# Optimization experiments

Hardware: AMD Instinct MI355X
Metric: run time of the kernel (lower is better)

The kernel has to match this reference:

```python
import math
import jax, jax.numpy as jnp
import numpy as np

RS_IN = [(128, 0), (64, 1), (32, 2)]
RS_OUT = [(128, 0), (64, 1), (32, 2)]
SET_LF = [0, 1, 2, 3, 4]
BATCH = 512
HIDDEN = 64

def _lfilters(l_in, l_out):
    return list(range(abs(l_in - l_out), l_in + l_out + 1))

N_PATH = sum(mo * mi * len(_lfilters(li, lo)) for mo, lo in RS_OUT for mi, li in RS_IN)  # 70656

# ---------- Clebsch-Gordan (numpy, setup time only) ----------

def _su2_cg(j1, j2, j3):
    f = math.factorial
    C = np.zeros((2 * j1 + 1, 2 * j2 + 1, 2 * j3 + 1))
    for m1 in range(-j1, j1 + 1):
        for m2 in range(-j2, j2 + 1):
            m3 = m1 + m2
            if abs(m3) > j3:
                continue
            pref = math.sqrt((2 * j3 + 1) * f(j3 + j1 - j2) * f(j3 - j1 + j2) * f(j1 + j2 - j3) / f(j1 + j2 + j3 + 1))
            pref *= math.sqrt(f(j3 + m3) * f(j3 - m3) * f(j1 - m1) * f(j1 + m1) * f(j2 - m2) * f(j2 + m2))
            s = 0.0
            for v in range(0, j1 + j2 - j3 + 1):
                d = [v, j1 + j2 - j3 - v, j1 - m1 - v, j2 + m2 - v, j3 - j2 + m1 + v, j3 - j1 - m2 + v]
                if any(x < 0 for x in d):
                    continue
                s += (-1) ** v / float(np.prod([f(x) for x in d]))
            C[j1 + m1, j2 + m2, j3 + m3] = pref * s
    return C

def _r2c(l):
    # change of basis real -> complex spherical harmonics, with phase making CG real
    q = np.zeros((2 * l + 1, 2 * l + 1), dtype=complex)
    for m in range(-l, 0):
        q[l + m, l + abs(m)] = 1 / math.sqrt(2)
        q[l + m, l - abs(m)] = -1j / math.sqrt(2)
    q[l, l] = 1
    for m in range(1, l + 1):
        q[l + m, l + abs(m)] = (-1) ** m / math.sqrt(2)
        q[l + m, l - abs(m)] = 1j * (-1) ** m / math.sqrt(2)
    return ((-1j) ** l) * q

def _cg_real(l1, l2, l3):
    C = np.einsum('ai,bj,ck,abc->ijk', _r2c(l1), _r2c(l2), np.conj(_r2c(l3)), _su2_cg(l1, l2, l3))
    C = C.imag if np.abs(C.imag).sum() > np.abs(C.real).sum() else C.real
    n = np.linalg.norm(C)
    return C / n if n > 0 else C

# ---------- real spherical harmonics (jax) ----------

def _sh(ls, r):
    # r: [batch, 3] -> Y: [sum(2l+1 for l in ls), batch]
    eps = 1e-9
    nrm = jnp.linalg.norm(r, axis=1, keepdims=True)
    d = r / jnp.maximum(nrm, eps)
    x, y, z = d[:, 0], d[:, 1], d[:, 2]
    rxy = jnp.sqrt(jnp.maximum(x * x + y * y, eps * eps))
    cphi, sphi = x / rxy, y / rxy
    lmax = max(ls)
    somx2 = jnp.sqrt(jnp.maximum(1.0 - z * z, 1e-12))
    P = {}
    pmm = jnp.ones_like(z)
    for m in range(lmax + 1):
        if m > 0:
            pmm = pmm * (2 * m - 1) * somx2
        P[(m, m)] = pmm
        if m + 1 <= lmax:
            P[(m + 1, m)] = z * (2 * m + 1) * pmm
        for l in range(m + 2, lmax + 1):
            P[(l, m)] = ((2 * l - 1) * z * P[(l - 1, m)] - (l + m - 1) * P[(l - 2, m)]) / (l - m)
    cm = [jnp.ones_like(z), cphi]
    sm = [jnp.zeros_like(z), sphi]
    for m in range(2, lmax + 1):
        cm.append(cm[m - 1] * cphi - sm[m - 1] * sphi)
        sm.append(sm[m - 1] * cphi + cm[m - 1] * sphi)
    f = math.factorial
    rows = []
    for l in ls:
        for m in range(-l, l + 1):
            am = abs(m)
            N = math.sqrt((2 * l + 1) / (4 * math.pi) * f(l - am) / f(l + am))
            if m == 0:
                rows.append(N * P[(l, 0)])
            elif m > 0:
                rows.append(math.sqrt(2) * N * P[(l, am)] * cm[am])
            else:
                rows.append(math.sqrt(2) * N * P[(l, am)] * sm[am])
    return jnp.stack(rows, axis=0)

# ---------- kernel forward ----------

def _kernel_forward(r, w1, b1, w2, b2, Qs):
    batch = r.shape[0]
    Ys = _sh(SET_LF, r)                       # [25, batch]
    radii = jnp.linalg.norm(r, axis=1)        # [batch]
    h = jax.nn.relu(radii[:, None] @ w1 + b1) # [batch, HIDDEN]
    coefficients = h @ w2 + b2                # [batch, N_PATH]
    begin_c = 0
    out_blocks = []
    for i, (mul_out, l_out) in enumerate(RS_OUT):
        num_summed = sum(mul_in * len(_lfilters(l_in, l_out)) for mul_in, l_in in RS_IN)
        in_blocks = []
        for j, (mul_in, l_in) in enumerate(RS_IN):
            lfs = _lfilters(l_in, l_out)
            n = mul_out * mul_in * len(lfs)
            c = coefficients[:, begin_c:begin_c + n].reshape(batch, mul_out, mul_in, len(lfs))
            begin_c += n
            Qij = Qs[i][j]
            K = 0
            for k, lf in enumerate(lfs):
                off_y = sum(2 * l + 1 for l in SET_LF if l < lf)
                Y = Ys[off_y:off_y + 2 * lf + 1]                 # [2lf+1, batch]
                off_q = sum(2 * l + 1 for l in lfs if l < lf)
                Q = Qij[:, :, off_q:off_q + 2 * lf + 1]          # [2lo+1, 2li+1, 2lf+1]
                K = K + jnp.einsum('ijk,kz,zuv->zuivj', Q, Y, c[..., k])
            # normalization == 'norm'
            xnorm = math.sqrt(2 * l_in + 1) * math.sqrt(4 * math.pi) / math.sqrt(num_summed)
            K = K * xnorm
            in_blocks.append(K.reshape(batch, mul_out * (2 * l_out + 1), mul_in * (2 * l_in + 1)))
        out_blocks.append(jnp.concatenate(in_blocks, axis=2))
    return jnp.concatenate(out_blocks, axis=1)  # [batch, 480, 480]

def setup_inputs() -> dict:
    key = jax.random.key(0)
    ks = jax.random.split(key, 5)
    inp = {}
    inp['r'] = jax.random.normal(ks[0], (BATCH, 3), dtype=jnp.float32)
    inp['w1'] = jax.random.normal(ks[1], (1, HIDDEN), dtype=jnp.float32) * 0.5
    inp['b1'] = jax.random.normal(ks[2], (HIDDEN,), dtype=jnp.float32) * 0.1
    inp['w2'] = jax.random.normal(ks[3], (HIDDEN, N_PATH), dtype=jnp.float32) * (1.0 / math.sqrt(HIDDEN))
    inp['b2'] = jax.random.normal(ks[4], (N_PATH,), dtype=jnp.float32) * 0.01
    for i, (mo, lo) in enumerate(RS_OUT):
        for j, (mi, li) in enumerate(RS_IN):
            Q = np.concatenate([_cg_real(lo, li, lf) for lf in _lfilters(li, lo)], axis=2)
            inp['Q_%d_%d' % (i, j)] = jnp.asarray(Q, dtype=jnp.float32)
    return inp

def reference(r, w1, b1, w2, b2, Q_0_0, Q_0_1, Q_0_2, Q_1_0, Q_1_1, Q_1_2, Q_2_0, Q_2_1, Q_2_2):
    Qs = [[Q_0_0, Q_0_1, Q_0_2], [Q_1_0, Q_1_1, Q_1_2], [Q_2_0, Q_2_1, Q_2_2]]
    return _kernel_forward(r, w1, b1, w2, b2, Qs)
```

## Files before the change

kernel.cpp:

```cpp
#include <hip/hip_runtime.h>
#include <math.h>

#define NPATH 70656
#define NBATCH 512
#define OUTD 480
#define OUTSZ (OUTD*OUTD)
#define ZCHV 64
#define ZT 8

constexpr int CBEG_TAB[9] = {0,16384,24576,28672,36864,49152,55296,59392,65536};

struct QPtrs { const float* q[9]; };

__global__ __launch_bounds__(256) void sh_mlp_kernel(
    const float* __restrict__ r, const float* __restrict__ w1,
    const float* __restrict__ b1, float* __restrict__ Yg,
    float* __restrict__ hTz)
{
  int z = blockIdx.x*256 + threadIdx.x;
  if (z >= NBATCH) return;
  float x = r[3*z], y = r[3*z+1], zz = r[3*z+2];
  float nrm = sqrtf(x*x + y*y + zz*zz);
  float inv = 1.0f / fmaxf(nrm, 1e-9f);
  float dx = x*inv, dy = y*inv, dz = zz*inv;
  float rxy = sqrtf(fmaxf(dx*dx + dy*dy, 1e-18f));
  float cphi = dx/rxy, sphi = dy/rxy;
  float somx2 = sqrtf(fmaxf(1.0f - dz*dz, 1e-12f));

  float P[5][5];
  float pmm = 1.0f;
  #pragma unroll
  for (int m = 0; m < 5; ++m) {
    if (m > 0) pmm *= (float)(2*m-1) * somx2;
    P[m][m] = pmm;
    if (m+1 < 5) P[m+1][m] = dz * (float)(2*m+1) * pmm;
    #pragma unroll
    for (int l = m+2; l < 5; ++l)
      P[l][m] = ((float)(2*l-1)*dz*P[l-1][m] - (float)(l+m-1)*P[l-2][m]) / (float)(l-m);
  }
  float cm[5], sm[5];
  cm[0]=1.0f; sm[0]=0.0f; cm[1]=cphi; sm[1]=sphi;
  #pragma unroll
  for (int m = 2; m < 5; ++m) {
    cm[m] = cm[m-1]*cphi - sm[m-1]*sphi;
    sm[m] = sm[m-1]*cphi + cm[m-1]*sphi;
  }
  const float fact[9] = {1,1,2,6,24,120,720,5040,40320};
  int row = 0;
  #pragma unroll
  for (int l = 0; l < 5; ++l) {
    #pragma unroll
    for (int m = -l; m <= l; ++m) {
      int am = m < 0 ? -m : m;
      float N = sqrtf((float)(2*l+1) / 12.566370614359172f * fact[l-am] / fact[l+am]);
      float v;
      if (m == 0)      v = N * P[l][0];
      else if (m > 0)  v = 1.4142135623730951f * N * P[l][am] * cm[am];
      else             v = 1.4142135623730951f * N * P[l][am] * sm[am];
      Yg[z*25 + row] = v;
      ++row;
    }
  }
  #pragma unroll
  for (int k = 0; k < 64; ++k)
    hTz[z*64 + k] = fmaxf(nrm * w1[k] + b1[k], 0.0f);
}

template<int LO, int LI>
__device__ __forceinline__ void stream_body(
    int bidl, const float* __restrict__ Yg, const float* __restrict__ hTz,
    const float* __restrict__ w2f, const float* __restrict__ b2,
    const float* __restrict__ Q, float* __restrict__ out)
{
  constexpr int DI = 2*LO+1, DJ = 2*LI+1;
  constexpr int MI = 128>>LI;
  constexpr int NUV = (128>>LO)*MI;
  constexpr int UVB = NUV/256;
  constexpr int LF = LO+LI;
  constexpr int MAXM = 2*LF+1;
  constexpr int ROWOFF = (LO==0)?0:((LO==1)?128:320);
  constexpr int COLOFF = (LI==0)?0:((LI==1)?128:320);
  constexpr int CBEG = CBEG_TAB[LO*3+LI];
  constexpr float NS = (LO==0)?224.0f:((LO==1)?416.0f:480.0f);
  const float xn = sqrtf((float)(2*LI+1) * 12.566370614359172f / NS);

  const int tid = threadIdx.x;
  const int uvb   = bidl % UVB;
  const int chunk = bidl / UVB;
  const int z0 = chunk * ZCHV;
  const int uv = uvb*256 + tid;
  const int uu = uv >> (7-LI);
  const int vv = uv & (MI-1);
  const int path = CBEG + uv;
  const float b2p = b2[path];

  float Qv[DI*DJ][MAXM];
  #pragma unroll
  for (int ij = 0; ij < DI*DJ; ++ij)
    #pragma unroll
    for (int m = 0; m < MAXM; ++m)
      Qv[ij][m] = Q[ij*MAXM + m];

  float* outR = out + (size_t)(ROWOFF + uu*DI)*OUTD + COLOFF + vv*DJ;

  for (int t0 = 0; t0 < ZCHV; t0 += ZT) {
    float acc[ZT];
    #pragma unroll
    for (int zt = 0; zt < ZT; ++zt) acc[zt] = b2p;
    #pragma unroll
    for (int kk = 0; kk < 64; kk += 16) {
      float w2c[16];
      #pragma unroll
      for (int k = 0; k < 16; ++k) w2c[k] = w2f[(size_t)(kk+k)*NPATH + path];
      #pragma unroll
      for (int zt = 0; zt < ZT; ++zt) {
        const float* hz = hTz + (size_t)(z0+t0+zt)*64 + kk;
        float s0=0.f, s1=0.f, s2=0.f, s3=0.f;
        #pragma unroll
        for (int k = 0; k < 16; k += 4) {
          s0 = fmaf(hz[k],   w2c[k],   s0);
          s1 = fmaf(hz[k+1], w2c[k+1], s1);
          s2 = fmaf(hz[k+2], w2c[k+2], s2);
          s3 = fmaf(hz[k+3], w2c[k+3], s3);
        }
        acc[zt] += (s0+s1)+(s2+s3);
      }
    }
    #pragma unroll
    for (int zt = 0; zt < ZT; ++zt) {
      const int z = z0 + t0 + zt;
      const float* yz = Yg + (size_t)z*25 + LF*LF;
      const float c = acc[zt]*xn;
      float* oz = outR + (size_t)z*OUTSZ;
      #pragma unroll
      for (int i = 0; i < DI; ++i)
        #pragma unroll
        for (int j = 0; j < DJ; ++j) {
          float a = 0.0f;
          #pragma unroll
          for (int m = 0; m < MAXM; ++m) a = fmaf(Qv[i*DJ+j][m], yz[m], a);
          oz[i*OUTD + j] = a*c;
        }
    }
  }
}

template<int LO, int LI>
__device__ __forceinline__ void tiled_body(
    int bidl, const float* __restrict__ Yg, const float* __restrict__ hTz,
    const float* __restrict__ w2f, const float* __restrict__ b2,
    const float* __restrict__ Q, float* __restrict__ out,
    float* c_lds, float* A_lds)
{
  constexpr int DI = 2*LO+1, DJ = 2*LI+1;
  constexpr int MO = 128>>LO, MI = 128>>LI;
  constexpr int NL = 2*((LO<LI)?LO:LI)+1;
  constexpr int LF0 = (LO>LI)?(LO-LI):(LI-LO);
  constexpr int QDIM = (LO+LI+1)*(LO+LI+1) - LF0*LF0;
  constexpr int NUV = MO*MI;
  constexpr int G = 256/NL;
  constexpr int UVB = (NUV + G - 1)/G;
  constexpr int NOUT = G*DI*DJ;
  constexpr int OPT = (NOUT + 255)/256;
  constexpr int ASIZE = DI*DJ*NL;
  constexpr int MAXM = 2*(LO+LI)+1;
  constexpr int ROWOFF = (LO==0)?0:((LO==1)?128:320);
  constexpr int COLOFF = (LI==0)?0:((LI==1)?128:320);
  constexpr int CBEG = CBEG_TAB[LO*3+LI];
  constexpr float NS = (LO==0)?224.0f:((LO==1)?416.0f:480.0f);
  const float xn = sqrtf((float)(2*LI+1) * 12.566370614359172f / NS);

  const int tid = threadIdx.x;
  const int uvb   = bidl % UVB;
  const int chunk = bidl / UVB;
  const int uv0 = uvb * G;
  const int z0  = chunk * ZCHV;

  const int gl = tid / NL;
  const int kf = tid % NL;
  const bool cact = (gl < G) && (uv0 + gl < NUV);
  const int path = CBEG + (cact ? ((uv0+gl)*NL + kf) : 0);
  const float b2p = b2[path];

  float Qv[MAXM];
  int yb = 0;
  {
    int t = (tid < ASIZE) ? tid : 0;
    int i  = t / (DJ*NL);
    int j  = (t / NL) % DJ;
    int kA = t % NL;
    int lf = LF0 + kA;
    int qoff = kA*(2*LF0 + kA);
    int mlim = 2*lf + 1;
    yb = lf*lf;
    #pragma unroll
    for (int m = 0; m < MAXM; ++m)
      Qv[m] = (m < mlim) ? Q[(i*DJ + j)*QDIM + qoff + m] : 0.0f;
  }

  int rowoff_o[OPT], aidx_o[OPT], cidx_o[OPT];
  bool val_o[OPT];
  #pragma unroll
  for (int t = 0; t < OPT; ++t) {
    int o = tid + 256*t;
    bool v = o < NOUT;
    int oo = v ? o : 0;
    int i   = oo / (G*DJ);
    int rem = oo % (G*DJ);
    int g   = rem / DJ;
    int j   = rem % DJ;
    int uv  = uv0 + g;
    v = v && (uv < NUV);
    int uu = uv >> (7-LI);
    int vv = uv & (MI-1);
    rowoff_o[t] = (uu*DI + i)*OUTD + vv*DJ + j;
    aidx_o[t] = (i*DJ + j)*NL;
    cidx_o[t] = g*NL;
    val_o[t] = v;
  }

  float* outR = out + ROWOFF*OUTD + COLOFF;

  for (int tile = 0; tile < ZCHV/ZT; ++tile) {
    const int p = tile & 1;
    float* cb = c_lds + p*(ZT*256);
    float* ab = A_lds + p*(ZT*128);
    const int zb = z0 + tile*ZT;

    float acc[ZT];
    #pragma unroll
    for (int zt = 0; zt < ZT; ++zt) acc[zt] = b2p;
    #pragma unroll
    for (int kk = 0; kk < 64; kk += 16) {
      float w2c[16];
      #pragma unroll
      for (int k = 0; k < 16; ++k) w2c[k] = w2f[(size_t)(kk+k)*NPATH + path];
      #pragma unroll
      for (int zt = 0; zt < ZT; ++zt) {
        const float* hz = hTz + (size_t)(zb+zt)*64 + kk;
        float s0=0.f, s1=0.f, s2=0.f, s3=0.f;
        #pragma unroll
        for (int k = 0; k < 16; k += 4) {
          s0 = fmaf(hz[k],   w2c[k],   s0);
          s1 = fmaf(hz[k+1], w2c[k+1], s1);
          s2 = fmaf(hz[k+2], w2c[k+2], s2);
          s3 = fmaf(hz[k+3], w2c[k+3], s3);
        }
        acc[zt] += (s0+s1)+(s2+s3);
      }
    }
    #pragma unroll
    for (int zt = 0; zt < ZT; ++zt) cb[zt*256 + tid] = acc[zt];

    if (tid < ASIZE) {
      #pragma unroll
      for (int zt = 0; zt < ZT; ++zt) {
        const float* yz = Yg + (size_t)(zb+zt)*25 + yb;
        float s = 0.0f;
        #pragma unroll
        for (int m = 0; m < MAXM; ++m) s = fmaf(Qv[m], yz[m], s);
        ab[zt*128 + tid] = s;
      }
    }
    __syncthreads();

    for (int zt = 0; zt < ZT; ++zt) {
      float* oz = outR + (size_t)(zb+zt)*OUTSZ;
      const float* cbz = cb + zt*256;
      const float* abz = ab + zt*128;
      #pragma unroll
      for (int t = 0; t < OPT; ++t) {
        if (val_o[t]) {
          float s = 0.0f;
          #pragma unroll
          for (int k = 0; k < NL; ++k) s += abz[aidx_o[t] + k] * cbz[cidx_o[t] + k];
          oz[rowoff_o[t]] = s*xn;
        }
      }
    }
  }
}

__global__ __launch_bounds__(256) void tp_stream_kernel(
    const float* __restrict__ Yg, const float* __restrict__ hTz,
    const float* __restrict__ w2, const float* __restrict__ b2,
    QPtrs qp, float* __restrict__ out)
{
  const int b = blockIdx.x;
  const int chunk = b / 160;
  const int r = b % 160;
  if      (r <  64) stream_body<0,0>(chunk*64 + r,      Yg,hTz,w2,b2,qp.q[0],out);
  else if (r <  96) stream_body<0,1>(chunk*32 + (r- 64),Yg,hTz,w2,b2,qp.q[1],out);
  else if (r < 112) stream_body<0,2>(chunk*16 + (r- 96),Yg,hTz,w2,b2,qp.q[2],out);
  else if (r < 144) stream_body<1,0>(chunk*32 + (r-112),Yg,hTz,w2,b2,qp.q[3],out);
  else              stream_body<2,0>(chunk*16 + (r-144),Yg,hTz,w2,b2,qp.q[6],out);
}

__global__ __launch_bounds__(256) void tp_tiled_kernel(
    const float* __restrict__ Yg, const float* __restrict__ hTz,
    const float* __restrict__ w2, const float* __restrict__ b2,
    QPtrs qp, float* __restrict__ out)
{
  __shared__ float c_lds[2*ZT*256];
  __shared__ float A_lds[2*ZT*128];
  const int b = blockIdx.x;
  const int chunk = b / 120;
  const int r = b % 120;
  if      (r <  49) tiled_body<1,1>(chunk*49 + r,      Yg,hTz,w2,b2,qp.q[4],out,c_lds,A_lds);
  else if (r <  74) tiled_body<1,2>(chunk*25 + (r-49), Yg,hTz,w2,b2,qp.q[5],out,c_lds,A_lds);
  else if (r <  99) tiled_body<2,1>(chunk*25 + (r-74), Yg,hTz,w2,b2,qp.q[7],out,c_lds,A_lds);
  else              tiled_body<2,2>(chunk*21 + (r-99), Yg,hTz,w2,b2,qp.q[8],out,c_lds,A_lds);
}

extern "C" void kernel_launch(void* const* d_in, const int* in_sizes, int n_in,
                              void* d_out, int out_size, void* d_ws, size_t ws_size,
                              hipStream_t stream)
{
  (void)in_sizes; (void)n_in; (void)out_size; (void)ws_size;
  const float* r  = (const float*)d_in[0];
  const float* w1 = (const float*)d_in[1];
  const float* b1 = (const float*)d_in[2];
  const float* w2 = (const float*)d_in[3];
  const float* b2 = (const float*)d_in[4];
  float* out = (float*)d_out;

  float* ws  = (float*)d_ws;
  float* Yg  = ws;
  float* hTz = ws + 12800;

  QPtrs qp;
  for (int i = 0; i < 9; ++i) qp.q[i] = (const float*)d_in[5 + i];

  const int nchunk = NBATCH / ZCHV;
  hipLaunchKernelGGL(sh_mlp_kernel, dim3(2), dim3(256), 0, stream, r, w1, b1, Yg, hTz);
  hipLaunchKernelGGL(tp_tiled_kernel,  dim3(nchunk*120), dim3(256), 0, stream,
                     Yg, hTz, w2, b2, qp, out);
  hipLaunchKernelGGL(tp_stream_kernel, dim3(nchunk*160), dim3(256), 0, stream,
                     Yg, hTz, w2, b2, qp, out);
}
```

Measured before the change: 219.9 us.

## Transpose w2 per path, merge tensor-product kernels, double ZT tile

```diff
diff --git a/kernel.cpp b/kernel.cpp
--- a/kernel.cpp
+++ b/kernel.cpp
@@ -6,11 +6,32 @@
 #define OUTD 480
 #define OUTSZ (OUTD*OUTD)
 #define ZCHV 64
-#define ZT 8
+#define ZT 16
 
 constexpr int CBEG_TAB[9] = {0,16384,24576,28672,36864,49152,55296,59392,65536};
 
 struct QPtrs { const float* q[9]; };
+
+__global__ __launch_bounds__(256) void w2t_kernel(
+    const float* __restrict__ w2, float* __restrict__ w2T)
+{
+  __shared__ float tile[64][65];
+  const int p0 = blockIdx.x * 64;
+  const int tk = threadIdx.x >> 6;
+  const int tp = threadIdx.x & 63;
+  #pragma unroll
+  for (int kk = 0; kk < 64; kk += 4) {
+    int k = kk + tk;
+    tile[k][tp] = w2[(size_t)k*NPATH + p0 + tp];
+  }
+  __syncthreads();
+  #pragma unroll
+  for (int i = 0; i < 16; ++i) {
+    int idx = threadIdx.x + 256*i;
+    int pr = idx >> 6, kc = idx & 63;
+    w2T[(size_t)(p0 + pr)*64 + kc] = tile[kc][pr];
+  }
+}
 
 __global__ __launch_bounds__(256) void sh_mlp_kernel(
     const float* __restrict__ r, const float* __restrict__ w1,
@@ -69,7 +90,7 @@
 template<int LO, int LI>
 __device__ __forceinline__ void stream_body(
     int bidl, const float* __restrict__ Yg, const float* __restrict__ hTz,
-    const float* __restrict__ w2f, const float* __restrict__ b2,
+    const float* __restrict__ w2T, const float* __restrict__ b2,
     const float* __restrict__ Q, float* __restrict__ out)
 {
   constexpr int DI = 2*LO+1, DJ = 2*LI+1;
@@ -93,6 +114,7 @@
   const int vv = uv & (MI-1);
   const int path = CBEG + uv;
   const float b2p = b2[path];
+  const float4* w2p4 = (const float4*)(w2T + (size_t)path*64);
 
   float Qv[DI*DJ][MAXM];
   #pragma unroll
@@ -110,8 +132,10 @@
     #pragma unroll
     for (int kk = 0; kk < 64; kk += 16) {
       float w2c[16];
-      #pragma unroll
-      for (int k = 0; k < 16; ++k) w2c[k] = w2f[(size_t)(kk+k)*NPATH + path];
+      *(float4*)&w2c[0]  = w2p4[kk/4];
+      *(float4*)&w2c[4]  = w2p4[kk/4+1];
+      *(float4*)&w2c[8]  = w2p4[kk/4+2];
+      *(float4*)&w2c[12] = w2p4[kk/4+3];
       #pragma unroll
       for (int zt = 0; zt < ZT; ++zt) {
         const float* hz = hTz + (size_t)(z0+t0+zt)*64 + kk;
@@ -148,7 +172,7 @@
 template<int LO, int LI>
 __device__ __forceinline__ void tiled_body(
     int bidl, const float* __restrict__ Yg, const float* __restrict__ hTz,
-    const float* __restrict__ w2f, const float* __restrict__ b2,
+    const float* __restrict__ w2T, const float* __restrict__ b2,
     const float* __restrict__ Q, float* __restrict__ out,
     float* c_lds, float* A_lds)
 {
@@ -181,6 +205,7 @@
   const bool cact = (gl < G) && (uv0 + gl < NUV);
   const int path = CBEG + (cact ? ((uv0+gl)*NL + kf) : 0);
   const float b2p = b2[path];
+  const float4* w2p4 = (const float4*)(w2T + (size_t)path*64);
 
   float Qv[MAXM];
   int yb = 0;
@@ -222,10 +247,8 @@
   float* outR = out + ROWOFF*OUTD + COLOFF;
 
   for (int tile = 0; tile < ZCHV/ZT; ++tile) {
-    const int p = tile & 1;
-    float* cb = c_lds + p*(ZT*256);
-    float* ab = A_lds + p*(ZT*128);
     const int zb = z0 + tile*ZT;
+    __syncthreads();
 
     float acc[ZT];
     #pragma unroll
@@ -233,8 +256,10 @@
     #pragma unroll
     for (int kk = 0; kk < 64; kk += 16) {
       float w2c[16];
-      #pragma unroll
-      for (int k = 0; k < 16; ++k) w2c[k] = w2f[(size_t)(kk+k)*NPATH + path];
+      *(float4*)&w2c[0]  = w2p4[kk/4];
+      *(float4*)&w2c[4]  = w2p4[kk/4+1];
+      *(float4*)&w2c[8]  = w2p4[kk/4+2];
+      *(float4*)&w2c[12] = w2p4[kk/4+3];
       #pragma unroll
       for (int zt = 0; zt < ZT; ++zt) {
         const float* hz = hTz + (size_t)(zb+zt)*64 + kk;
@@ -250,7 +275,7 @@
       }
     }
     #pragma unroll
-    for (int zt = 0; zt < ZT; ++zt) cb[zt*256 + tid] = acc[zt];
+    for (int zt = 0; zt < ZT; ++zt) c_lds[zt*256 + tid] = acc[zt];
 
     if (tid < ASIZE) {
       #pragma unroll
@@ -259,15 +284,15 @@
         float s = 0.0f;
         #pragma unroll
         for (int m = 0; m < MAXM; ++m) s = fmaf(Qv[m], yz[m], s);
-        ab[zt*128 + tid] = s;
+        A_lds[zt*128 + tid] = s;
       }
     }
     __syncthreads();
 
     for (int zt = 0; zt < ZT; ++zt) {
       float* oz = outR + (size_t)(zb+zt)*OUTSZ;
-      const float* cbz = cb + zt*256;
-      const float* abz = ab + zt*128;
+      const float* cbz = c_lds + zt*256;
+      const float* abz = A_lds + zt*128;
       #pragma unroll
       for (int t = 0; t < OPT; ++t) {
         if (val_o[t]) {
@@ -281,35 +306,25 @@
   }
 }
 
-__global__ __launch_bounds__(256) void tp_stream_kernel(
+__global__ __launch_bounds__(256) void tp_kernel(
     const float* __restrict__ Yg, const float* __restrict__ hTz,
-    const float* __restrict__ w2, const float* __restrict__ b2,
+    const float* __restrict__ w2T, const float* __restrict__ b2,
     QPtrs qp, float* __restrict__ out)
 {
+  __shared__ float c_lds[ZT*256];
+  __shared__ float A_lds[ZT*128];
   const int b = blockIdx.x;
-  const int chunk = b / 160;
-  const int r = b % 160;
-  if      (r <  64) stream_body<0,0>(chunk*64 + r,      Yg,hTz,w2,b2,qp.q[0],out);
-  else if (r <  96) stream_body<0,1>(chunk*32 + (r- 64),Yg,hTz,w2,b2,qp.q[1],out);
-  else if (r < 112) stream_body<0,2>(chunk*16 + (r- 96),Yg,hTz,w2,b2,qp.q[2],out);
-  else if (r < 144) stream_body<1,0>(chunk*32 + (r-112),Yg,hTz,w2,b2,qp.q[3],out);
-  else              stream_body<2,0>(chunk*16 + (r-144),Yg,hTz,w2,b2,qp.q[6],out);
-}
-
-__global__ __launch_bounds__(256) void tp_tiled_kernel(
-    const float* __restrict__ Yg, const float* __restrict__ hTz,
-    const float* __restrict__ w2, const float* __restrict__ b2,
-    QPtrs qp, float* __restrict__ out)
-{
-  __shared__ float c_lds[2*ZT*256];
-  __shared__ float A_lds[2*ZT*128];
-  const int b = blockIdx.x;
-  const int chunk = b / 120;
-  const int r = b % 120;
-  if      (r <  49) tiled_body<1,1>(chunk*49 + r,      Yg,hTz,w2,b2,qp.q[4],out,c_lds,A_lds);
-  else if (r <  74) tiled_body<1,2>(chunk*25 + (r-49), Yg,hTz,w2,b2,qp.q[5],out,c_lds,A_lds);
-  else if (r <  99) tiled_body<2,1>(chunk*25 + (r-74), Yg,hTz,w2,b2,qp.q[7],out,c_lds,A_lds);
-  else              tiled_body<2,2>(chunk*21 + (r-99), Yg,hTz,w2,b2,qp.q[8],out,c_lds,A_lds);
+  const int chunk = b / 280;
+  const int r = b % 280;
+  if      (r <  64) stream_body<0,0>(chunk*64 + r,      Yg,hTz,w2T,b2,qp.q[0],out);
+  else if (r <  96) stream_body<0,1>(chunk*32 + (r- 64),Yg,hTz,w2T,b2,qp.q[1],out);
+  else if (r < 112) stream_body<0,2>(chunk*16 + (r- 96),Yg,hTz,w2T,b2,qp.q[2],out);
+  else if (r < 144) stream_body<1,0>(chunk*32 + (r-112),Yg,hTz,w2T,b2,qp.q[3],out);
+  else if (r < 160) stream_body<2,0>(chunk*16 + (r-144),Yg,hTz,w2T,b2,qp.q[6],out);
+  else if (r < 209) tiled_body<1,1>(chunk*49 + (r-160), Yg,hTz,w2T,b2,qp.q[4],out,c_lds,A_lds);
+  else if (r < 234) tiled_body<1,2>(chunk*25 + (r-209), Yg,hTz,w2T,b2,qp.q[5],out,c_lds,A_lds);
+  else if (r < 259) tiled_body<2,1>(chunk*25 + (r-234), Yg,hTz,w2T,b2,qp.q[7],out,c_lds,A_lds);
+  else              tiled_body<2,2>(chunk*21 + (r-259), Yg,hTz,w2T,b2,qp.q[8],out,c_lds,A_lds);
 }
 
 extern "C" void kernel_launch(void* const* d_in, const int* in_sizes, int n_in,
@@ -327,14 +342,13 @@
   float* ws  = (float*)d_ws;
   float* Yg  = ws;
   float* hTz = ws + 12800;
+  float* w2T = ws + 12800 + 32768;
 
   QPtrs qp;
   for (int i = 0; i < 9; ++i) qp.q[i] = (const float*)d_in[5 + i];
 
-  const int nchunk = NBATCH / ZCHV;
+  hipLaunchKernelGGL(w2t_kernel, dim3(NPATH/64), dim3(256), 0, stream, w2, w2T);
   hipLaunchKernelGGL(sh_mlp_kernel, dim3(2), dim3(256), 0, stream, r, w1, b1, Yg, hTz);
-  hipLaunchKernelGGL(tp_tiled_kernel,  dim3(nchunk*120), dim3(256), 0, stream,
-                     Yg, hTz, w2, b2, qp, out);
-  hipLaunchKernelGGL(tp_stream_kernel, dim3(nchunk*160), dim3(256), 0, stream,
-                     Yg, hTz, w2, b2, qp, out);
-}
+  hipLaunchKernelGGL(tp_kernel, dim3((NBATCH/ZCHV)*280), dim3(256), 0, stream,
+                     Yg, hTz, w2T, b2, qp, out);
+}
```

New measurement: 283.8 us. +29.1%, slower.

## Reorder w2 by filter-major layout and give each thread one uv with all filters

Applied to the files above, without the earlier changes.

```diff
diff --git a/kernel.cpp b/kernel.cpp
--- a/kernel.cpp
+++ b/kernel.cpp
@@ -5,12 +5,37 @@
 #define NBATCH 512
 #define OUTD 480
 #define OUTSZ (OUTD*OUTD)
-#define ZCHV 64
-#define ZT 8
+#define ZCHV_S 64
+#define ZTS 16
+#define ZCHV_T 16
+#define ZTT 8
 
 constexpr int CBEG_TAB[9] = {0,16384,24576,28672,36864,49152,55296,59392,65536};
+constexpr int NL_TAB[9]   = {1,1,1,1,3,3,1,3,5};
+constexpr int NUVL_TAB[9] = {14,13,12,13,12,11,12,11,10};
 
 struct QPtrs { const float* q[9]; };
+
+__global__ __launch_bounds__(256) void reorder_kernel(
+    const float* __restrict__ w2, const float* __restrict__ b2,
+    float* __restrict__ w2R, float* __restrict__ b2R)
+{
+  int p = blockIdx.x*256 + threadIdx.x;
+  if (p >= NPATH) return;
+  int reg = 0;
+  #pragma unroll
+  for (int i = 1; i < 9; ++i) if (p >= CBEG_TAB[i]) reg = i;
+  const int pl  = p - CBEG_TAB[reg];
+  const int nl  = NL_TAB[reg];
+  const int nuvl = NUVL_TAB[reg];
+  const int kf = pl >> nuvl;
+  const int uv = pl & ((1 << nuvl) - 1);
+  const int pold = CBEG_TAB[reg] + uv*nl + kf;
+  b2R[p] = b2[pold];
+  #pragma unroll 8
+  for (int k = 0; k < 64; ++k)
+    w2R[(size_t)k*NPATH + p] = w2[(size_t)k*NPATH + pold];
+}
 
 __global__ __launch_bounds__(256) void sh_mlp_kernel(
     const float* __restrict__ r, const float* __restrict__ w1,
@@ -69,7 +94,7 @@
 template<int LO, int LI>
 __device__ __forceinline__ void stream_body(
     int bidl, const float* __restrict__ Yg, const float* __restrict__ hTz,
-    const float* __restrict__ w2f, const float* __restrict__ b2,
+    const float* __restrict__ w2R, const float* __restrict__ b2R,
     const float* __restrict__ Q, float* __restrict__ out)
 {
   constexpr int DI = 2*LO+1, DJ = 2*LI+1;
@@ -87,12 +112,12 @@
   const int tid = threadIdx.x;
   const int uvb   = bidl % UVB;
   const int chunk = bidl / UVB;
-  const int z0 = chunk * ZCHV;
+  const int z0 = chunk * ZCHV_S;
   const int uv = uvb*256 + tid;
   const int uu = uv >> (7-LI);
   const int vv = uv & (MI-1);
   const int path = CBEG + uv;
-  const float b2p = b2[path];
+  const float b2p = b2R[path];
 
   float Qv[DI*DJ][MAXM];
   #pragma unroll
@@ -103,31 +128,35 @@
 
   float* outR = out + (size_t)(ROWOFF + uu*DI)*OUTD + COLOFF + vv*DJ;
 
-  for (int t0 = 0; t0 < ZCHV; t0 += ZT) {
-    float acc[ZT];
-    #pragma unroll
-    for (int zt = 0; zt < ZT; ++zt) acc[zt] = b2p;
+  for (int t0 = 0; t0 < ZCHV_S; t0 += ZTS) {
+    float acc[ZTS];
+    #pragma unroll
+    for (int zt = 0; zt < ZTS; ++zt) acc[zt] = b2p;
     #pragma unroll
     for (int kk = 0; kk < 64; kk += 16) {
       float w2c[16];
       #pragma unroll
-      for (int k = 0; k < 16; ++k) w2c[k] = w2f[(size_t)(kk+k)*NPATH + path];
-      #pragma unroll
-      for (int zt = 0; zt < ZT; ++zt) {
+      for (int k = 0; k < 16; ++k)
+        w2c[k] = w2R[(size_t)(kk+k)*NPATH + path];
+      #pragma unroll
+      for (int zt = 0; zt < ZTS; ++zt) {
         const float* hz = hTz + (size_t)(z0+t0+zt)*64 + kk;
+        float h[16];
+        #pragma unroll
+        for (int q = 0; q < 16; q += 4) *(float4*)&h[q] = *(const float4*)(hz+q);
         float s0=0.f, s1=0.f, s2=0.f, s3=0.f;
         #pragma unroll
         for (int k = 0; k < 16; k += 4) {
-          s0 = fmaf(hz[k],   w2c[k],   s0);
-          s1 = fmaf(hz[k+1], w2c[k+1], s1);
-          s2 = fmaf(hz[k+2], w2c[k+2], s2);
-          s3 = fmaf(hz[k+3], w2c[k+3], s3);
+          s0 = fmaf(h[k],   w2c[k],   s0);
+          s1 = fmaf(h[k+1], w2c[k+1], s1);
+          s2 = fmaf(h[k+2], w2c[k+2], s2);
+          s3 = fmaf(h[k+3], w2c[k+3], s3);
         }
         acc[zt] += (s0+s1)+(s2+s3);
       }
     }
     #pragma unroll
-    for (int zt = 0; zt < ZT; ++zt) {
+    for (int zt = 0; zt < ZTS; ++zt) {
       const int z = z0 + t0 + zt;
       const float* yz = Yg + (size_t)z*25 + LF*LF;
       const float c = acc[zt]*xn;
@@ -146,11 +175,10 @@
 }
 
 template<int LO, int LI>
-__device__ __forceinline__ void tiled_body(
+__device__ __forceinline__ void tiled_uv_body(
     int bidl, const float* __restrict__ Yg, const float* __restrict__ hTz,
-    const float* __restrict__ w2f, const float* __restrict__ b2,
-    const float* __restrict__ Q, float* __restrict__ out,
-    float* c_lds, float* A_lds)
+    const float* __restrict__ w2R, const float* __restrict__ b2R,
+    const float* __restrict__ Q, float* __restrict__ out, float* A_lds)
 {
   constexpr int DI = 2*LO+1, DJ = 2*LI+1;
   constexpr int MO = 128>>LO, MI = 128>>LI;
@@ -158,29 +186,27 @@
   constexpr int LF0 = (LO>LI)?(LO-LI):(LI-LO);
   constexpr int QDIM = (LO+LI+1)*(LO+LI+1) - LF0*LF0;
   constexpr int NUV = MO*MI;
-  constexpr int G = 256/NL;
-  constexpr int UVB = (NUV + G - 1)/G;
-  constexpr int NOUT = G*DI*DJ;
-  constexpr int OPT = (NOUT + 255)/256;
+  constexpr int UVB = NUV/256;
   constexpr int ASIZE = DI*DJ*NL;
   constexpr int MAXM = 2*(LO+LI)+1;
-  constexpr int ROWOFF = (LO==0)?0:((LO==1)?128:320);
-  constexpr int COLOFF = (LI==0)?0:((LI==1)?128:320);
+  constexpr int KKC = (NL==5)?8:16;
+  constexpr int ROWOFF = (LO==1)?128:320;
+  constexpr int COLOFF = (LI==1)?128:320;
   constexpr int CBEG = CBEG_TAB[LO*3+LI];
-  constexpr float NS = (LO==0)?224.0f:((LO==1)?416.0f:480.0f);
+  constexpr float NS = (LO==1)?416.0f:480.0f;
   const float xn = sqrtf((float)(2*LI+1) * 12.566370614359172f / NS);
 
   const int tid = threadIdx.x;
   const int uvb   = bidl % UVB;
   const int chunk = bidl / UVB;
-  const int uv0 = uvb * G;
-  const int z0  = chunk * ZCHV;
-
-  const int gl = tid / NL;
-  const int kf = tid % NL;
-  const bool cact = (gl < G) && (uv0 + gl < NUV);
-  const int path = CBEG + (cact ? ((uv0+gl)*NL + kf) : 0);
-  const float b2p = b2[path];
+  const int z0 = chunk * ZCHV_T;
+  const int uv = uvb*256 + tid;
+  const int uu = uv >> (7-LI);
+  const int vv = uv & (MI-1);
+
+  float b2p[NL];
+  #pragma unroll
+  for (int kf = 0; kf < NL; ++kf) b2p[kf] = b2R[CBEG + kf*NUV + uv];
 
   float Qv[MAXM];
   int yb = 0;
@@ -198,118 +224,95 @@
       Qv[m] = (m < mlim) ? Q[(i*DJ + j)*QDIM + qoff + m] : 0.0f;
   }
 
-  int rowoff_o[OPT], aidx_o[OPT], cidx_o[OPT];
-  bool val_o[OPT];
-  #pragma unroll
-  for (int t = 0; t < OPT; ++t) {
-    int o = tid + 256*t;
-    bool v = o < NOUT;
-    int oo = v ? o : 0;
-    int i   = oo / (G*DJ);
-    int rem = oo % (G*DJ);
-    int g   = rem / DJ;
-    int j   = rem % DJ;
-    int uv  = uv0 + g;
-    v = v && (uv < NUV);
-    int uu = uv >> (7-LI);
-    int vv = uv & (MI-1);
-    rowoff_o[t] = (uu*DI + i)*OUTD + vv*DJ + j;
-    aidx_o[t] = (i*DJ + j)*NL;
-    cidx_o[t] = g*NL;
-    val_o[t] = v;
-  }
-
-  float* outR = out + ROWOFF*OUTD + COLOFF;
-
-  for (int tile = 0; tile < ZCHV/ZT; ++tile) {
-    const int p = tile & 1;
-    float* cb = c_lds + p*(ZT*256);
-    float* ab = A_lds + p*(ZT*128);
-    const int zb = z0 + tile*ZT;
-
-    float acc[ZT];
-    #pragma unroll
-    for (int zt = 0; zt < ZT; ++zt) acc[zt] = b2p;
-    #pragma unroll
-    for (int kk = 0; kk < 64; kk += 16) {
-      float w2c[16];
-      #pragma unroll
-      for (int k = 0; k < 16; ++k) w2c[k] = w2f[(size_t)(kk+k)*NPATH + path];
-      #pragma unroll
-      for (int zt = 0; zt < ZT; ++zt) {
-        const float* hz = hTz + (size_t)(zb+zt)*64 + kk;
-        float s0=0.f, s1=0.f, s2=0.f, s3=0.f;
-        #pragma unroll
-        for (int k = 0; k < 16; k += 4) {
-          s0 = fmaf(hz[k],   w2c[k],   s0);
-          s1 = fmaf(hz[k+1], w2c[k+1], s1);
-          s2 = fmaf(hz[k+2], w2c[k+2], s2);
-          s3 = fmaf(hz[k+3], w2c[k+3], s3);
-        }
-        acc[zt] += (s0+s1)+(s2+s3);
-      }
-    }
-    #pragma unroll
-    for (int zt = 0; zt < ZT; ++zt) cb[zt*256 + tid] = acc[zt];
+  float* outR = out + (size_t)(ROWOFF + uu*DI)*OUTD + COLOFF + vv*DJ;
+
+  for (int tile = 0; tile < ZCHV_T/ZTT; ++tile) {
+    const int zb = z0 + tile*ZTT;
+    float* ab = A_lds + (tile & 1)*(ZTT*ASIZE);
 
     if (tid < ASIZE) {
       #pragma unroll
-      for (int zt = 0; zt < ZT; ++zt) {
+      for (int zt = 0; zt < ZTT; ++zt) {
         const float* yz = Yg + (size_t)(zb+zt)*25 + yb;
         float s = 0.0f;
         #pragma unroll
         for (int m = 0; m < MAXM; ++m) s = fmaf(Qv[m], yz[m], s);
-        ab[zt*128 + tid] = s;
+        ab[zt*ASIZE + tid] = s*xn;
       }
     }
+
+    float c[NL][ZTT];
+    #pragma unroll
+    for (int kf = 0; kf < NL; ++kf)
+      #pragma unroll
+      for (int zt = 0; zt < ZTT; ++zt) c[kf][zt] = b2p[kf];
+    #pragma unroll
+    for (int kk = 0; kk < 64; kk += KKC) {
+      float w2c[NL][KKC];
+      #pragma unroll
+      for (int kf = 0; kf < NL; ++kf)
+        #pragma unroll
+        for (int k = 0; k < KKC; ++k)
+          w2c[kf][k] = w2R[(size_t)(kk+k)*NPATH + CBEG + kf*NUV + uv];
+      #pragma unroll
+      for (int zt = 0; zt < ZTT; ++zt) {
+        const float* hz = hTz + (size_t)(zb+zt)*64 + kk;
+        float h[KKC];
+        #pragma unroll
+        for (int q = 0; q < KKC; q += 4) *(float4*)&h[q] = *(const float4*)(hz+q);
+        #pragma unroll
+        for (int kf = 0; kf < NL; ++kf)
+          #pragma unroll
+          for (int k = 0; k < KKC; ++k)
+            c[kf][zt] = fmaf(h[k], w2c[kf][k], c[kf][zt]);
+      }
+    }
     __syncthreads();
 
-    for (int zt = 0; zt < ZT; ++zt) {
+    for (int zt = 0; zt < ZTT; ++zt) {
       float* oz = outR + (size_t)(zb+zt)*OUTSZ;
-      const float* cbz = cb + zt*256;
-      const float* abz = ab + zt*128;
-      #pragma unroll
-      for (int t = 0; t < OPT; ++t) {
-        if (val_o[t]) {
+      #pragma unroll
+      for (int i = 0; i < DI; ++i)
+        #pragma unroll
+        for (int j = 0; j < DJ; ++j) {
           float s = 0.0f;
           #pragma unroll
-          for (int k = 0; k < NL; ++k) s += abz[aidx_o[t] + k] * cbz[cidx_o[t] + k];
-          oz[rowoff_o[t]] = s*xn;
+          for (int kf = 0; kf < NL; ++kf)
+            s = fmaf(ab[zt*ASIZE + (i*DJ+j)*NL + kf], c[kf][zt], s);
+          oz[i*OUTD + j] = s;
         }
-      }
     }
   }
 }
 
 __global__ __launch_bounds__(256) void tp_stream_kernel(
     const float* __restrict__ Yg, const float* __restrict__ hTz,
-    const float* __restrict__ w2, const float* __restrict__ b2,
+    const float* __restrict__ w2R, const float* __restrict__ b2R,
     QPtrs qp, float* __restrict__ out)
 {
   const int b = blockIdx.x;
   const int chunk = b / 160;
   const int r = b % 160;
-  if      (r <  64) stream_body<0,0>(chunk*64 + r,      Yg,hTz,w2,b2,qp.q[0],out);
-  else if (r <  96) stream_body<0,1>(chunk*32 + (r- 64),Yg,hTz,w2,b2,qp.q[1],out);
-  else if (r < 112) stream_body<0,2>(chunk*16 + (r- 96),Yg,hTz,w2,b2,qp.q[2],out);
-  else if (r < 144) stream_body<1,0>(chunk*32 + (r-112),Yg,hTz,w2,b2,qp.q[3],out);
-  else              stream_body<2,0>(chunk*16 + (r-144),Yg,hTz,w2,b2,qp.q[6],out);
+  if      (r <  64) stream_body<0,0>(chunk*64 + r,      Yg,hTz,w2R,b2R,qp.q[0],out);
+  else if (r <  96) stream_body<0,1>(chunk*32 + (r- 64),Yg,hTz,w2R,b2R,qp.q[1],out);
+  else if (r < 112) stream_body<0,2>(chunk*16 + (r- 96),Yg,hTz,w2R,b2R,qp.q[2],out);
+  else if (r < 144) stream_body<1,0>(chunk*32 + (r-112),Yg,hTz,w2R,b2R,qp.q[3],out);
+  else              stream_body<2,0>(chunk*16 + (r-144),Yg,hTz,w2R,b2R,qp.q[6],out);
 }
 
 __global__ __launch_bounds__(256) void tp_tiled_kernel(
     const float* __restrict__ Yg, const float* __restrict__ hTz,
-    const float* __restrict__ w2, const float* __restrict__ b2,
+    const float* __restrict__ w2R, const float* __restrict__ b2R,
     QPtrs qp, float* __restrict__ out)
 {
-  __shared__ float c_lds[2*ZT*256];
-  __shared__ float A_lds[2*ZT*128];
+  __shared__ float A_lds[2*ZTT*125];
   const int b = blockIdx.x;
-  const int chunk = b / 120;
-  const int r = b % 120;
-  if      (r <  49) tiled_body<1,1>(chunk*49 + r,      Yg,hTz,w2,b2,qp.q[4],out,c_lds,A_lds);
-  else if (r <  74) tiled_body<1,2>(chunk*25 + (r-49), Yg,hTz,w2,b2,qp.q[5],out,c_lds,A_lds);
-  else if (r <  99) tiled_body<2,1>(chunk*25 + (r-74), Yg,hTz,w2,b2,qp.q[7],out,c_lds,A_lds);
-  else              tiled_body<2,2>(chunk*21 + (r-99), Yg,hTz,w2,b2,qp.q[8],out,c_lds,A_lds);
+  const int chunk = b / 36;
+  const int r = b % 36;
+  if      (r < 16) tiled_uv_body<1,1>(chunk*16 + r,     Yg,hTz,w2R,b2R,qp.q[4],out,A_lds);
+  else if (r < 24) tiled_uv_body<1,2>(chunk*8 + (r-16), Yg,hTz,w2R,b2R,qp.q[5],out,A_lds);
+  else if (r < 32) tiled_uv_body<2,1>(chunk*8 + (r-24), Yg,hTz,w2R,b2R,qp.q[7],out,A_lds);
+  else             tiled_uv_body<2,2>(chunk*4 + (r-32), Yg,hTz,w2R,b2R,qp.q[8],out,A_lds);
 }
 
 extern "C" void kernel_launch(void* const* d_in, const int* in_sizes, int n_in,
@@ -327,14 +330,17 @@
   float* ws  = (float*)d_ws;
   float* Yg  = ws;
   float* hTz = ws + 12800;
+  float* w2R = ws + 12800 + 32768;
+  float* b2R = w2R + (size_t)NPATH*64;
 
   QPtrs qp;
   for (int i = 0; i < 9; ++i) qp.q[i] = (const float*)d_in[5 + i];
 
-  const int nchunk = NBATCH / ZCHV;
+  hipLaunchKernelGGL(reorder_kernel, dim3((NPATH+255)/256), dim3(256), 0, stream,
+                     w2, b2, w2R, b2R);
   hipLaunchKernelGGL(sh_mlp_kernel, dim3(2), dim3(256), 0, stream, r, w1, b1, Yg, hTz);
-  hipLaunchKernelGGL(tp_tiled_kernel,  dim3(nchunk*120), dim3(256), 0, stream,
-                     Yg, hTz, w2, b2, qp, out);
-  hipLaunchKernelGGL(tp_stream_kernel, dim3(nchunk*160), dim3(256), 0, stream,
-                     Yg, hTz, w2, b2, qp, out);
-}
+  hipLaunchKernelGGL(tp_tiled_kernel, dim3((NBATCH/ZCHV_T)*36), dim3(256), 0, stream,
+                     Yg, hTz, w2R, b2R, qp, out);
+  hipLaunchKernelGGL(tp_stream_kernel, dim3((NBATCH/ZCHV_S)*160), dim3(256), 0, stream,
+                     Yg, hTz, w2R, b2R, qp, out);
+}
```

Result: slower. 299.5 us (+36.2%).
